# Kernel tuning notes

Measured on AMD Instinct MI355X. Metric: run time of the kernel, lower is better.

## Reference

```python
import jax, jax.numpy as jnp
import numpy as np

MAX_DEPTH = 10
N_CLASSES = 10
N_FEATURES = 16
MAX_NODES = 2 ** (MAX_DEPTH + 1) - 1  # 2047
N_INTERNAL = 2 ** MAX_DEPTH - 1       # 1023; nodes [N_INTERNAL, MAX_NODES) are leaves
N_SAMPLES = 4_000_000


def setup_inputs() -> dict:
    key = jax.random.key(0)
    k_x, k_f, k_t, k_v = jax.random.split(key, 4)
    X = jax.random.normal(k_x, (N_SAMPLES, N_FEATURES), dtype=jnp.float32)

    idx = jnp.arange(MAX_NODES)
    is_internal = idx < N_INTERNAL
    # complete binary tree: children of internal node i are 2i+1, 2i+2; leaves point to self
    tree_left = jnp.where(is_internal, 2 * idx + 1, idx).astype(jnp.int32)
    tree_right = jnp.where(is_internal, 2 * idx + 2, idx).astype(jnp.int32)
    tree_is_leaf = ~is_internal
    tree_feature = jnp.where(
        is_internal,
        jax.random.randint(k_f, (MAX_NODES,), 0, N_FEATURES),
        0,
    ).astype(jnp.int32)
    # thresholds ~ N(0,1) match the N(0,1) features, giving balanced splits
    tree_threshold = jax.random.normal(k_t, (MAX_NODES,), dtype=jnp.float32)
    # leaf class-count distributions (as stored by _make_leaf)
    tree_value = jax.random.uniform(k_v, (MAX_NODES, N_CLASSES), dtype=jnp.float32) * 100.0
    return {
        "X": X,
        "tree_feature": tree_feature,
        "tree_threshold": tree_threshold,
        "tree_left": tree_left,
        "tree_right": tree_right,
        "tree_value": tree_value,
        "tree_is_leaf": tree_is_leaf,
    }


def reference(X, tree_feature, tree_threshold, tree_left, tree_right, tree_value, tree_is_leaf):
    # Vectorized level-synchronous tree traversal (same math as the torch forward's
    # while-loop: every sample steps down one level per iteration, freezing once it
    # reaches a leaf; output is tree_value at the reached leaf).
    n = X.shape[0]
    node0 = jnp.zeros((n,), dtype=jnp.int32)

    def step(_, node):
        feat = tree_feature[node]                      # [n]
        thr = tree_threshold[node]                     # [n]
        xv = jnp.take_along_axis(X, feat[:, None], axis=1)[:, 0]  # [n]
        nxt = jnp.where(xv <= thr, tree_left[node], tree_right[node])
        return jnp.where(tree_is_leaf[node], node, nxt)

    node = jax.lax.fori_loop(0, MAX_DEPTH, step, node0)
    return tree_value[node]                            # [n, n_classes]
```

## Files before the change

### kernel.cpp

```cpp
#include <hip/hip_runtime.h>


#define BLOCK 256
#define SPT   5

constexpr int kFeat     = 16;
constexpr int kCls      = 10;
constexpr int kDepth    = 10;
constexpr int kInternal = 1023;
constexpr int kNS       = BLOCK * SPT;
constexpr int kOutVec4  = kNS * kCls / 4;

typedef float fx4 __attribute__((ext_vector_type(4)));
typedef float fx2 __attribute__((ext_vector_type(2)));

struct FT { int feat; float thr; };

__device__ __forceinline__ float sel16(fx4 a, fx4 b, fx4 c, fx4 d, int f) {
    const bool b0 = f & 1, b1 = f & 2, b2 = f & 4, b3 = f & 8;
    float a01 = b0 ? a.y : a.x, a23 = b0 ? a.w : a.z;
    float b01 = b0 ? b.y : b.x, b23 = b0 ? b.w : b.z;
    float c01 = b0 ? c.y : c.x, c23 = b0 ? c.w : c.z;
    float d01 = b0 ? d.y : d.x, d23 = b0 ? d.w : d.z;
    float av = b1 ? a23 : a01, bv = b1 ? b23 : b01;
    float cv = b1 ? c23 : c01, dv = b1 ? d23 : d01;
    float ab = b2 ? bv : av,   cd = b2 ? dv : cv;
    return b3 ? cd : ab;
}

__global__ __launch_bounds__(BLOCK) void dtree_kernel(
    const float* __restrict__ X,
    const int*   __restrict__ tfeat,
    const float* __restrict__ tthr,
    const float* __restrict__ tval,
    float*       __restrict__ out,
    int n)
{
    __shared__ FT  s_node[kInternal + 1];
    __shared__ int s_leafnode[kNS];

    const int tid = threadIdx.x;
    const long long base = (long long)blockIdx.x * kNS;
    const bool fullblk = (base + kNS <= (long long)n);

    fx4 xr[SPT][4];
    #pragma unroll
    for (int s = 0; s < SPT; ++s) {
        const long long smp = base + (long long)s * BLOCK + tid;
        if (fullblk || smp < (long long)n) {
            const fx4* xp = reinterpret_cast<const fx4*>(X) + smp * 4;
            xr[s][0] = __builtin_nontemporal_load(xp + 0);
            xr[s][1] = __builtin_nontemporal_load(xp + 1);
            xr[s][2] = __builtin_nontemporal_load(xp + 2);
            xr[s][3] = __builtin_nontemporal_load(xp + 3);
        } else {
            xr[s][0] = xr[s][1] = xr[s][2] = xr[s][3] = (fx4)(0.f);
        }
    }

    for (int i = tid; i < kInternal; i += BLOCK) {
        FT nd; nd.feat = tfeat[i]; nd.thr = tthr[i];
        s_node[i] = nd;
    }
    __syncthreads();

    int node[SPT];
    #pragma unroll
    for (int s = 0; s < SPT; ++s) node[s] = 0;

    #pragma unroll
    for (int d = 0; d < kDepth; ++d) {
        FT nd[SPT];
        #pragma unroll
        for (int s = 0; s < SPT; ++s) nd[s] = s_node[node[s]];
        #pragma unroll
        for (int s = 0; s < SPT; ++s) {
            const float x = sel16(xr[s][0], xr[s][1], xr[s][2], xr[s][3], nd[s].feat);
            node[s] = 2 * node[s] + 1 + ((x <= nd[s].thr) ? 0 : 1);
        }
    }

    #pragma unroll
    for (int s = 0; s < SPT; ++s)
        s_leafnode[s * BLOCK + tid] = node[s];
    __syncthreads();

    float* gout = out + base * kCls;
    if (fullblk) {
        for (int j = tid; j < kOutVec4; j += BLOCK) {
            const int sib = (2 * j) / 5;
            const int c0  = 4 * j - 10 * sib;
            const bool span = (c0 == 8);
            const int sib1 = span ? sib + 1 : sib;
            const int off1 = span ? 0 : c0 + 2;
            const long long n0 = s_leafnode[sib];
            const long long n1 = s_leafnode[sib1];
            const fx2 u0 = *reinterpret_cast<const fx2*>(tval + n0 * kCls + c0);
            const fx2 u1 = *reinterpret_cast<const fx2*>(tval + n1 * kCls + off1);
            fx4 v; v.x = u0.x; v.y = u0.y; v.z = u1.x; v.w = u1.y;
            __builtin_nontemporal_store(v, reinterpret_cast<fx4*>(gout) + j);
        }
    } else {
        const long long nsValid = (long long)n - base;
        const long long fvalid  = (nsValid > 0 ? nsValid : 0) * kCls;
        for (long long f = tid; f < fvalid; f += BLOCK) {
            const long long sib = f / kCls;
            const int c = (int)(f - sib * kCls);
            gout[f] = tval[(long long)s_leafnode[sib] * kCls + c];
        }
    }
}

extern "C" void kernel_launch(void* const* d_in, const int* in_sizes, int n_in,
                              void* d_out, int out_size, void* d_ws, size_t ws_size,
                              hipStream_t stream) {
    const float* X     = (const float*)d_in[0];
    const int*   tfeat = (const int*)d_in[1];
    const float* tthr  = (const float*)d_in[2];
    const float* tval  = (const float*)d_in[5];
    float* out = (float*)d_out;

    const int n = in_sizes[0] / kFeat;
    const int grid = (n + kNS - 1) / kNS;
    dtree_kernel<<<grid, BLOCK, 0, stream>>>(X, tfeat, tthr, tval, out, n);
}
```

Before: 429.2 us.

## Stage X tiles into LDS via direct global-to-LDS loads, one sample per thread

Each block now handles 256 samples with one sample per thread instead of 5. The X rows and tree tables are copied straight into shared memory with global_load_lds, and each traversal step reads the chosen feature from LDS instead of running a 16-way register select. Output stores change from 16-byte nontemporal writes to plain 8-byte writes. This cuts register pressure and the select ALU work, at the cost of more blocks, repeated tree-table loads per block, and LDS bank traffic during traversal.

```diff
diff --git a/kernel.cpp b/kernel.cpp
--- a/kernel.cpp
+++ b/kernel.cpp
@@ -1,31 +1,21 @@
 #include <hip/hip_runtime.h>
+#include <stdint.h>
 
 
 #define BLOCK 256
-#define SPT   5
 
 constexpr int kFeat     = 16;
 constexpr int kCls      = 10;
 constexpr int kDepth    = 10;
 constexpr int kInternal = 1023;
-constexpr int kNS       = BLOCK * SPT;
-constexpr int kOutVec4  = kNS * kCls / 4;
 
-typedef float fx4 __attribute__((ext_vector_type(4)));
 typedef float fx2 __attribute__((ext_vector_type(2)));
 
-struct FT { int feat; float thr; };
-
-__device__ __forceinline__ float sel16(fx4 a, fx4 b, fx4 c, fx4 d, int f) {
-    const bool b0 = f & 1, b1 = f & 2, b2 = f & 4, b3 = f & 8;
-    float a01 = b0 ? a.y : a.x, a23 = b0 ? a.w : a.z;
-    float b01 = b0 ? b.y : b.x, b23 = b0 ? b.w : b.z;
-    float c01 = b0 ? c.y : c.x, c23 = b0 ? c.w : c.z;
-    float d01 = b0 ? d.y : d.x, d23 = b0 ? d.w : d.z;
-    float av = b1 ? a23 : a01, bv = b1 ? b23 : b01;
-    float cv = b1 ? c23 : c01, dv = b1 ? d23 : d01;
-    float ab = b2 ? bv : av,   cd = b2 ? dv : cv;
-    return b3 ? cd : ab;
+__device__ __forceinline__ void gload16(const void* g, void* lds_base) {
+    __builtin_amdgcn_global_load_lds(
+        (const __attribute__((address_space(1))) void*)g,
+        (__attribute__((address_space(3))) void*)lds_base,
+        16, 0, 0);
 }
 
 __global__ __launch_bounds__(BLOCK) void dtree_kernel(
@@ -36,69 +26,60 @@
     float*       __restrict__ out,
     int n)
 {
-    __shared__ FT  s_node[kInternal + 1];
-    __shared__ int s_leafnode[kNS];
+    __shared__ float s_x[BLOCK * kFeat];
+    __shared__ int   s_feat[1024];
+    __shared__ float s_thr[1024];
+    __shared__ int   s_leaf[BLOCK];
 
-    const int tid = threadIdx.x;
-    const long long base = (long long)blockIdx.x * kNS;
-    const bool fullblk = (base + kNS <= (long long)n);
+    const int tid  = threadIdx.x;
+    const int lane = tid & 63;
+    const int w    = tid >> 6;
+    const long long base = (long long)blockIdx.x * BLOCK;
+    const bool fullblk = (base + BLOCK <= (long long)n);
 
-    fx4 xr[SPT][4];
-    #pragma unroll
-    for (int s = 0; s < SPT; ++s) {
-        const long long smp = base + (long long)s * BLOCK + tid;
-        if (fullblk || smp < (long long)n) {
-            const fx4* xp = reinterpret_cast<const fx4*>(X) + smp * 4;
-            xr[s][0] = __builtin_nontemporal_load(xp + 0);
-            xr[s][1] = __builtin_nontemporal_load(xp + 1);
-            xr[s][2] = __builtin_nontemporal_load(xp + 2);
-            xr[s][3] = __builtin_nontemporal_load(xp + 3);
-        } else {
-            xr[s][0] = xr[s][1] = xr[s][2] = xr[s][3] = (fx4)(0.f);
+    if (fullblk) {
+        gload16(tfeat + (w * 256 + 4 * lane), (char*)s_feat + w * 1024);
+        gload16(tthr  + (w * 256 + 4 * lane), (char*)s_thr  + w * 1024);
+
+        #pragma unroll
+        for (int i = 0; i < 4; ++i) {
+            const int s_local = w * 64 + i * 16 + (lane >> 2);
+            const float* src = X + (base + s_local) * kFeat + (lane & 3) * 4;
+            gload16(src, (char*)s_x + w * 4096 + i * 1024);
         }
-    }
-
-    for (int i = tid; i < kInternal; i += BLOCK) {
-        FT nd; nd.feat = tfeat[i]; nd.thr = tthr[i];
-        s_node[i] = nd;
+    } else {
+        for (int i = tid; i < 1024; i += BLOCK) {
+            s_feat[i] = tfeat[i];
+            s_thr[i]  = tthr[i];
+        }
+        const long long smp = base + tid;
+        if (smp < (long long)n)
+            for (int f = 0; f < kFeat; ++f)
+                s_x[tid * kFeat + f] = X[smp * kFeat + f];
     }
     __syncthreads();
 
-    int node[SPT];
-    #pragma unroll
-    for (int s = 0; s < SPT; ++s) node[s] = 0;
-
+    int node = 0;
     #pragma unroll
     for (int d = 0; d < kDepth; ++d) {
-        FT nd[SPT];
-        #pragma unroll
-        for (int s = 0; s < SPT; ++s) nd[s] = s_node[node[s]];
-        #pragma unroll
-        for (int s = 0; s < SPT; ++s) {
-            const float x = sel16(xr[s][0], xr[s][1], xr[s][2], xr[s][3], nd[s].feat);
-            node[s] = 2 * node[s] + 1 + ((x <= nd[s].thr) ? 0 : 1);
-        }
+        const int   f  = s_feat[node];
+        const float th = s_thr[node];
+        const float x  = s_x[tid * kFeat + f];
+        node = 2 * node + 1 + ((x <= th) ? 0 : 1);
     }
-
-    #pragma unroll
-    for (int s = 0; s < SPT; ++s)
-        s_leafnode[s * BLOCK + tid] = node[s];
+    s_leaf[tid] = node;
     __syncthreads();
 
     float* gout = out + base * kCls;
     if (fullblk) {
-        for (int j = tid; j < kOutVec4; j += BLOCK) {
-            const int sib = (2 * j) / 5;
-            const int c0  = 4 * j - 10 * sib;
-            const bool span = (c0 == 8);
-            const int sib1 = span ? sib + 1 : sib;
-            const int off1 = span ? 0 : c0 + 2;
-            const long long n0 = s_leafnode[sib];
-            const long long n1 = s_leafnode[sib1];
-            const fx2 u0 = *reinterpret_cast<const fx2*>(tval + n0 * kCls + c0);
-            const fx2 u1 = *reinterpret_cast<const fx2*>(tval + n1 * kCls + off1);
-            fx4 v; v.x = u0.x; v.y = u0.y; v.z = u1.x; v.w = u1.y;
-            __builtin_nontemporal_store(v, reinterpret_cast<fx4*>(gout) + j);
+        #pragma unroll
+        for (int k = 0; k < 5; ++k) {
+            const int j   = tid + k * BLOCK;
+            const int sib = j / 5;
+            const int c   = 2 * (j - 5 * sib);
+            const long long nd = s_leaf[sib];
+            const fx2 u = *reinterpret_cast<const fx2*>(tval + nd * kCls + c);
+            *reinterpret_cast<fx2*>(gout + 2 * j) = u;
         }
     } else {
         const long long nsValid = (long long)n - base;
@@ -106,7 +87,7 @@
         for (long long f = tid; f < fvalid; f += BLOCK) {
             const long long sib = f / kCls;
             const int c = (int)(f - sib * kCls);
-            gout[f] = tval[(long long)s_leafnode[sib] * kCls + c];
+            gout[f] = tval[(long long)s_leaf[sib] * kCls + c];
         }
     }
 }
@@ -121,6 +102,6 @@
     float* out = (float*)d_out;
 
     const int n = in_sizes[0] / kFeat;
-    const int grid = (n + kNS - 1) / kNS;
+    const int grid = (n + BLOCK - 1) / BLOCK;
     dtree_kernel<<<grid, BLOCK, 0, stream>>>(X, tfeat, tthr, tval, out, n);
 }
```

Result: faster. 393.1 us (-8.4%).
